# Performance work log

Hardware: AMD Instinct MI355X
Metric: run time of the kernel (lower is better)

Reference implementation:

```python
import jax, jax.numpy as jnp
import numpy as np
from jax import lax

N, C_IN, L = 32, 256, 4096
C_OUT, K, GROUPS = 256, 9, 4
C_DIM, PAD, STRIDE = 128, 4, 1


def setup_inputs() -> dict:
    key = jax.random.key(0)
    k1, k2, k3, k4, k5 = jax.random.split(key, 5)
    x = jax.random.normal(k1, (N, C_IN, L), dtype=jnp.float32)
    c = jax.random.normal(k2, (N, C_DIM), dtype=jnp.float32)
    weight = jax.random.normal(k3, (C_OUT, C_IN // GROUPS, K), dtype=jnp.float32)
    c_weight = jax.random.normal(k4, (C_OUT, C_DIM), dtype=jnp.float32)
    bias = jax.random.normal(k5, (C_OUT,), dtype=jnp.float32)
    return {"x": x, "c": c, "weight": weight, "c_weight": c_weight, "bias": bias}


def reference(x, c, weight, c_weight, bias):
    # Grouped conv1d: equivalent to the unfold+per-group matmul in the torch code.
    # dims: x (N, C_in, L), weight (C_out, C_in/groups, K) -> out (N, C_out, L_out)
    out = lax.conv_general_dilated(
        x, weight,
        window_strides=(STRIDE,),
        padding=[(PAD, PAD)],
        dimension_numbers=("NCH", "OIH", "NCH"),
        feature_group_count=GROUPS,
    )
    # Concat-path context: cat([patches, c]) @ cat([W, cW]).T == conv(x) + c @ cW.T,
    # with the context term broadcast over all temporal positions.
    ctx = jnp.einsum("nd,od->no", c, c_weight)  # (N, C_out)
    out = out + ctx[:, :, None] + bias[None, :, None]
    return out
```

## Files before the change

kernel.cpp:

```cpp
#include <hip/hip_runtime.h>
#include <hip/hip_bf16.h>

#define NB     32
#define CIN    256
#define LIN    4096
#define COUT   256
#define KW     9
#define NGRP   4
#define CDIM   128
#define CPG    64
#define LT     256
#define NROWS  264
#define RP     68
#define WF_ELEMS (4*4*9*2*64*8)

typedef __attribute__((ext_vector_type(8))) short short8;
typedef __attribute__((ext_vector_type(4))) short short4v;
typedef __attribute__((ext_vector_type(4))) float float4v;
typedef __attribute__((ext_vector_type(4))) unsigned short ushort4v;

__global__ void pack_weights(const float* __restrict__ w, __hip_bfloat16* __restrict__ wF) {
    int tid = blockIdx.x * blockDim.x + threadIdx.x;
    if (tid >= WF_ELEMS) return;
    int j    = tid & 7;
    int lane = (tid >> 3) & 63;
    int rest = tid >> 9;
    int chunk = rest & 1;  rest >>= 1;
    int k     = rest % 9;  rest /= 9;
    int co16  = rest & 3;
    int g     = rest >> 2;
    int co = g * CPG + co16 * 16 + (lane & 15);
    int ci = chunk * 32 + (lane >> 4) * 8 + j;
    wF[tid] = __float2bfloat16(w[(co * CPG + ci) * KW + k]);
}

__global__ __launch_bounds__(256) void ctx_kernel(const float* __restrict__ c,
                                                  const float* __restrict__ cw,
                                                  const float* __restrict__ bias,
                                                  float* __restrict__ ctxb) {
    int gw   = (blockIdx.x * 256 + threadIdx.x) >> 6;
    int lane = threadIdx.x & 63;
    int n  = gw >> 8;
    int co = gw & 255;
    float s = c[n * CDIM + lane]      * cw[co * CDIM + lane]
            + c[n * CDIM + 64 + lane] * cw[co * CDIM + 64 + lane];
    #pragma unroll
    for (int off = 32; off; off >>= 1) s += __shfl_down(s, off);
    if (lane == 0) ctxb[gw] = s + bias[co];
}

__global__ __launch_bounds__(256, 4) void conv_mfma(
    const float* __restrict__ x, const __hip_bfloat16* __restrict__ wF,
    const float* __restrict__ ctxb, float* __restrict__ out)
{
    __shared__ unsigned short sx[NROWS * RP];
    __shared__ float sctx[CPG];

    const int bx = blockIdx.x;
    const int t  = bx & 15;
    const int g  = (bx >> 4) & 3;
    const int n  = bx >> 6;
    const int l0 = t * LT;
    const int tid = threadIdx.x;
    const int lane = tid & 63;
    const int wv   = tid >> 6;

    if (tid < CPG) sctx[tid] = ctxb[n * COUT + g * CPG + tid];

    const float* xb = x + ((size_t)(n * CIN + g * CPG)) * LIN;

    {
        int q4  = 1 + (lane & 15);
        int cqb = 4 * wv + (lane >> 4);
        #pragma unroll
        for (int i = 0; i < 4; ++i, q4 += 16) {
            int lg = l0 - 4 + 4 * q4;
            float4v v[4];
            #pragma unroll
            for (int j = 0; j < 4; ++j)
                v[j] = *(const float4v*)(xb + (size_t)(4 * cqb + j) * LIN + lg);
            int row = 4 * q4;
            #pragma unroll
            for (int d = 0; d < 4; ++d) {
                ushort4v p;
                #pragma unroll
                for (int j = 0; j < 4; ++j)
                    p[j] = __builtin_bit_cast(unsigned short, __float2bfloat16(v[j][d]));
                *(ushort4v*)(&sx[(row + d) * RP + 4 * cqb]) = p;
            }
        }
    }
    if (tid < 32) {
        int head = (tid < 16);
        int q4 = head ? 0 : 65;
        int cq = tid & 15;
        int lg = l0 - 4 + 4 * q4;
        bool ok = head ? (t > 0) : (t < 15);
        float4v v[4];
        #pragma unroll
        for (int j = 0; j < 4; ++j)
            v[j] = ok ? *(const float4v*)(xb + (size_t)(4 * cq + j) * LIN + lg)
                      : (float4v){0.f, 0.f, 0.f, 0.f};
        int row = 4 * q4;
        #pragma unroll
        for (int d = 0; d < 4; ++d) {
            ushort4v p;
            #pragma unroll
            for (int j = 0; j < 4; ++j)
                p[j] = __builtin_bit_cast(unsigned short, __float2bfloat16(v[j][d]));
            *(ushort4v*)(&sx[(row + d) * RP + 4 * cq]) = p;
        }
    }
    __syncthreads();

    const int r  = lane & 15;
    const int q  = lane >> 4;
    const int wl = wv * 64;

    float4v acc[4][4];
    #pragma unroll
    for (int a = 0; a < 4; ++a)
        #pragma unroll
        for (int b = 0; b < 4; ++b)
            acc[a][b] = (float4v){0.f, 0.f, 0.f, 0.f};

    const short8* wFp = (const short8*)wF;

    #pragma unroll
    for (int k = 0; k < KW; ++k) {
        #pragma unroll
        for (int chunk = 0; chunk < 2; ++chunk) {
            short8 bfrag[4];
            #pragma unroll
            for (int l16 = 0; l16 < 4; ++l16) {
                int row = wl + l16 * 16 + r + k;
                int base = row * RP + chunk * 32 + q * 8;
                short4v lo = *(const short4v*)(&sx[base]);
                short4v hi = *(const short4v*)(&sx[base + 4]);
                bfrag[l16] = __builtin_shufflevector(lo, hi, 0, 1, 2, 3, 4, 5, 6, 7);
            }
            short8 afrag[4];
            #pragma unroll
            for (int co16 = 0; co16 < 4; ++co16) {
                afrag[co16] = wFp[(((g * 4 + co16) * 9 + k) * 2 + chunk) * 64 + lane];
            }
            #pragma unroll
            for (int co16 = 0; co16 < 4; ++co16)
                #pragma unroll
                for (int l16 = 0; l16 < 4; ++l16)
                    acc[co16][l16] = __builtin_amdgcn_mfma_f32_16x16x32_bf16(
                        afrag[co16], bfrag[l16], acc[co16][l16], 0, 0, 0);
        }
    }

    float* ob = out + ((size_t)(n * COUT + g * CPG)) * LIN + l0 + wl;
    #pragma unroll
    for (int co16 = 0; co16 < 4; ++co16) {
        #pragma unroll
        for (int reg = 0; reg < 4; ++reg) {
            int co_l = co16 * 16 + q * 4 + reg;
            float add = sctx[co_l];
            #pragma unroll
            for (int l16 = 0; l16 < 4; ++l16) {
                ob[(size_t)co_l * LIN + l16 * 16 + r] = acc[co16][l16][reg] + add;
            }
        }
    }
}

extern "C" void kernel_launch(void* const* d_in, const int* in_sizes, int n_in,
                              void* d_out, int out_size, void* d_ws, size_t ws_size,
                              hipStream_t stream) {
    const float* x    = (const float*)d_in[0];
    const float* c    = (const float*)d_in[1];
    const float* w    = (const float*)d_in[2];
    const float* cw   = (const float*)d_in[3];
    const float* bias = (const float*)d_in[4];
    float* out = (float*)d_out;

    __hip_bfloat16* wF = (__hip_bfloat16*)d_ws;
    float* ctxb = (float*)((char*)d_ws + (size_t)WF_ELEMS * 2);

    pack_weights<<<(WF_ELEMS + 255) / 256, 256, 0, stream>>>(w, wF);
    ctx_kernel<<<(NB * COUT * 64) / 256, 256, 0, stream>>>(c, cw, bias, ctxb);
    conv_mfma<<<NB * NGRP * (LIN / LT), 256, 0, stream>>>(x, wF, ctxb, out);
}
```

Measured before the change: 261.4 us.

## Software-pipeline x staging across channel chunks and two L-tiles per block

```diff
diff --git a/kernel.cpp b/kernel.cpp
--- a/kernel.cpp
+++ b/kernel.cpp
@@ -12,6 +12,7 @@
 #define LT     256
 #define NROWS  264
 #define RP     68
+#define TPB    2
 #define WF_ELEMS (4*4*9*2*64*8)
 
 typedef __attribute__((ext_vector_type(8))) short short8;
@@ -49,7 +50,7 @@
     if (lane == 0) ctxb[gw] = s + bias[co];
 }
 
-__global__ __launch_bounds__(256, 4) void conv_mfma(
+__global__ __launch_bounds__(256, 2) void conv_mfma(
     const float* __restrict__ x, const __hip_bfloat16* __restrict__ wF,
     const float* __restrict__ ctxb, float* __restrict__ out)
 {
@@ -57,10 +58,10 @@
     __shared__ float sctx[CPG];
 
     const int bx = blockIdx.x;
-    const int t  = bx & 15;
-    const int g  = (bx >> 4) & 3;
-    const int n  = bx >> 6;
-    const int l0 = t * LT;
+    const int pb = bx & 7;
+    const int g  = (bx >> 3) & 3;
+    const int n  = bx >> 5;
+    const int t0 = pb * TPB;
     const int tid = threadIdx.x;
     const int lane = tid & 63;
     const int wv   = tid >> 6;
@@ -69,53 +70,68 @@
 
     const float* xb = x + ((size_t)(n * CIN + g * CPG)) * LIN;
 
-    {
-        int q4  = 1 + (lane & 15);
-        int cqb = 4 * wv + (lane >> 4);
-        #pragma unroll
-        for (int i = 0; i < 4; ++i, q4 += 16) {
+    float4v rA[2][4], rB[2][4], rhA[4], rhB[4];
+
+    auto stage_load = [&](int c, int tg, float4v (&rm)[2][4], float4v (&rh)[4]) {
+        const int l0 = tg * LT;
+        #pragma unroll
+        for (int it = 0; it < 2; ++it) {
+            int cq = (lane >> 4) + 4 * it;
+            int q4 = 1 + (lane & 15) + 16 * wv;
             int lg = l0 - 4 + 4 * q4;
-            float4v v[4];
             #pragma unroll
             for (int j = 0; j < 4; ++j)
-                v[j] = *(const float4v*)(xb + (size_t)(4 * cqb + j) * LIN + lg);
+                rm[it][j] = *(const float4v*)(xb + (size_t)(32 * c + 4 * cq + j) * LIN + lg);
+        }
+        if (tid < 16) {
+            bool head = tid < 8;
+            int q4 = head ? 0 : 65;
+            int cq = tid & 7;
+            int lg = l0 - 4 + 4 * q4;
+            bool ok = head ? (tg > 0) : (tg < 15);
+            #pragma unroll
+            for (int j = 0; j < 4; ++j)
+                rh[j] = ok ? *(const float4v*)(xb + (size_t)(32 * c + 4 * cq + j) * LIN + lg)
+                           : (float4v){0.f, 0.f, 0.f, 0.f};
+        }
+    };
+
+    auto stage_write = [&](int c, float4v (&rm)[2][4], float4v (&rh)[4]) {
+        #pragma unroll
+        for (int it = 0; it < 2; ++it) {
+            int cq = (lane >> 4) + 4 * it;
+            int q4 = 1 + (lane & 15) + 16 * wv;
             int row = 4 * q4;
+            int colu = 4 * (8 * c + cq);
             #pragma unroll
             for (int d = 0; d < 4; ++d) {
                 ushort4v p;
                 #pragma unroll
                 for (int j = 0; j < 4; ++j)
-                    p[j] = __builtin_bit_cast(unsigned short, __float2bfloat16(v[j][d]));
-                *(ushort4v*)(&sx[(row + d) * RP + 4 * cqb]) = p;
-            }
-        }
-    }
-    if (tid < 32) {
-        int head = (tid < 16);
-        int q4 = head ? 0 : 65;
-        int cq = tid & 15;
-        int lg = l0 - 4 + 4 * q4;
-        bool ok = head ? (t > 0) : (t < 15);
-        float4v v[4];
-        #pragma unroll
-        for (int j = 0; j < 4; ++j)
-            v[j] = ok ? *(const float4v*)(xb + (size_t)(4 * cq + j) * LIN + lg)
-                      : (float4v){0.f, 0.f, 0.f, 0.f};
-        int row = 4 * q4;
-        #pragma unroll
-        for (int d = 0; d < 4; ++d) {
-            ushort4v p;
-            #pragma unroll
-            for (int j = 0; j < 4; ++j)
-                p[j] = __builtin_bit_cast(unsigned short, __float2bfloat16(v[j][d]));
-            *(ushort4v*)(&sx[(row + d) * RP + 4 * cq]) = p;
-        }
-    }
-    __syncthreads();
+                    p[j] = __builtin_bit_cast(unsigned short, __float2bfloat16(rm[it][j][d]));
+                *(ushort4v*)(&sx[(row + d) * RP + colu]) = p;
+            }
+        }
+        if (tid < 16) {
+            int q4 = (tid < 8) ? 0 : 65;
+            int cq = tid & 7;
+            int row = 4 * q4;
+            int colu = 4 * (8 * c + cq);
+            #pragma unroll
+            for (int d = 0; d < 4; ++d) {
+                ushort4v p;
+                #pragma unroll
+                for (int j = 0; j < 4; ++j)
+                    p[j] = __builtin_bit_cast(unsigned short, __float2bfloat16(rh[j][d]));
+                *(ushort4v*)(&sx[(row + d) * RP + colu]) = p;
+            }
+        }
+    };
 
     const int r  = lane & 15;
     const int q  = lane >> 4;
     const int wl = wv * 64;
+    const short8* wFp = (const short8*)wF;
 
     float4v acc[4][4];
     #pragma unroll
@@ -124,47 +140,70 @@
         for (int b = 0; b < 4; ++b)
             acc[a][b] = (float4v){0.f, 0.f, 0.f, 0.f};
 
-    const short8* wFp = (const short8*)wF;
-
-    #pragma unroll
-    for (int k = 0; k < KW; ++k) {
-        #pragma unroll
-        for (int chunk = 0; chunk < 2; ++chunk) {
+    auto compute_chunk = [&](int c) {
+        #pragma unroll
+        for (int k = 0; k < KW; ++k) {
             short8 bfrag[4];
             #pragma unroll
             for (int l16 = 0; l16 < 4; ++l16) {
                 int row = wl + l16 * 16 + r + k;
-                int base = row * RP + chunk * 32 + q * 8;
+                int base = row * RP + c * 32 + q * 8;
                 short4v lo = *(const short4v*)(&sx[base]);
                 short4v hi = *(const short4v*)(&sx[base + 4]);
                 bfrag[l16] = __builtin_shufflevector(lo, hi, 0, 1, 2, 3, 4, 5, 6, 7);
             }
-            short8 afrag[4];
             #pragma unroll
             for (int co16 = 0; co16 < 4; ++co16) {
-                afrag[co16] = wFp[(((g * 4 + co16) * 9 + k) * 2 + chunk) * 64 + lane];
-            }
-            #pragma unroll
-            for (int co16 = 0; co16 < 4; ++co16)
+                short8 af = wFp[(((g * 4 + co16) * 9 + k) * 2 + c) * 64 + lane];
                 #pragma unroll
                 for (int l16 = 0; l16 < 4; ++l16)
                     acc[co16][l16] = __builtin_amdgcn_mfma_f32_16x16x32_bf16(
-                        afrag[co16], bfrag[l16], acc[co16][l16], 0, 0, 0);
-        }
-    }
-
-    float* ob = out + ((size_t)(n * COUT + g * CPG)) * LIN + l0 + wl;
-    #pragma unroll
-    for (int co16 = 0; co16 < 4; ++co16) {
-        #pragma unroll
-        for (int reg = 0; reg < 4; ++reg) {
-            int co_l = co16 * 16 + q * 4 + reg;
-            float add = sctx[co_l];
-            #pragma unroll
-            for (int l16 = 0; l16 < 4; ++l16) {
-                ob[(size_t)co_l * LIN + l16 * 16 + r] = acc[co16][l16][reg] + add;
-            }
-        }
+                        af, bfrag[l16], acc[co16][l16], 0, 0, 0);
+            }
+        }
+    };
+
+    stage_load(0, t0, rA, rhA);
+    stage_load(1, t0, rB, rhB);
+    stage_write(0, rA, rhA);
+    __syncthreads();
+
+    #pragma unroll 1
+    for (int tt = 0; tt < TPB; ++tt) {
+        const int tg = t0 + tt;
+
+        compute_chunk(0);
+        stage_write(1, rB, rhB);
+        if (tt + 1 < TPB) stage_load(0, tg + 1, rA, rhA);
+        __syncthreads();
+
+        compute_chunk(1);
+
+        {
+            float* ob = out + ((size_t)(n * COUT + g * CPG)) * LIN + tg * LT + wl;
+            #pragma unroll
+            for (int co16 = 0; co16 < 4; ++co16) {
+                #pragma unroll
+                for (int rg = 0; rg < 4; ++rg) {
+                    int co_l = co16 * 16 + q * 4 + rg;
+                    float add = sctx[co_l];
+                    #pragma unroll
+                    for (int l16 = 0; l16 < 4; ++l16)
+                        ob[(size_t)co_l * LIN + l16 * 16 + r] = acc[co16][l16][rg] + add;
+                }
+            }
+            #pragma unroll
+            for (int a = 0; a < 4; ++a)
+                #pragma unroll
+                for (int b = 0; b < 4; ++b)
+                    acc[a][b] = (float4v){0.f, 0.f, 0.f, 0.f};
+        }
+
+        if (tt + 1 < TPB) {
+            stage_write(0, rA, rhA);
+            stage_load(1, tg + 1, rB, rhB);
+        }
+        __syncthreads();
     }
 }
 
@@ -183,5 +222,5 @@
 
     pack_weights<<<(WF_ELEMS + 255) / 256, 256, 0, stream>>>(w, wF);
     ctx_kernel<<<(NB * COUT * 64) / 256, 256, 0, stream>>>(c, cw, bias, ctxb);
-    conv_mfma<<<NB * NGRP * (LIN / LT), 256, 0, stream>>>(x, wF, ctxb, out);
-}
+    conv_mfma<<<NB * NGRP * (LIN / LT / TPB), 256, 0, stream>>>(x, wF, ctxb, out);
+}
```

New measurement: 485.9 us. 1.86x slower.
